# Kernel tuning notes

Hardware: AMD Instinct MI355X
Metric: run time of the kernel (lower is better)

The kernel has to match this reference:

```python
import jax, jax.numpy as jnp
import numpy as np

B, S, D = 8, 2048, 512

def setup_inputs() -> dict:
    key = jax.random.key(0)
    ks = jax.random.split(key, 9)
    sc = 1.0 / np.sqrt(D)
    return {
        "x": jax.random.normal(ks[0], (B, S, D), jnp.float32),
        "Wq": jax.random.normal(ks[1], (D, D), jnp.float32) * sc,
        "bq": jax.random.normal(ks[2], (D,), jnp.float32) * sc,
        "Wv": jax.random.normal(ks[3], (D, D), jnp.float32) * sc,
        "bv": jax.random.normal(ks[4], (D,), jnp.float32) * sc,
        "Wr": jax.random.normal(ks[5], (D, D), jnp.float32) * sc,
        "br": jax.random.normal(ks[6], (D,), jnp.float32) * sc,
        "Wl": jax.random.normal(ks[7], (1, D), jnp.float32) * sc,
        "bl": jax.random.normal(ks[8], (1,), jnp.float32) * sc,
    }

def reference(x, Wq, bq, Wv, bv, Wr, br, Wl, bl):
    # projections (torch Linear: x @ W.T + b)
    q = x @ Wq.T + bq          # [B,S,D]
    v = x @ Wv.T + bv          # [B,S,D]
    r = x @ Wr.T + br          # [B,S,D]
    # scores = Q @ V^T, softmax over dim=1 (the query/row axis!)
    scores = jnp.einsum("bsd,btd->bst", q, v)   # [B,S,S]
    attn = jax.nn.softmax(scores, axis=1)
    emb = jnp.einsum("bst,btd->bsd", attn, r)   # [B,S,D]
    pooled = emb.sum(axis=1)                    # [B,D]
    out = pooled @ Wl.T + bl                    # [B,1]
    return jax.nn.sigmoid(out)
```

## Files before the change

kernel.cpp:

```cpp
#include <hip/hip_runtime.h>
#include <math.h>

#define B 8
#define S 2048
#define D 512


#define CH 64
#define ROWS (S / CH)
#define DCH 32
#define DROWS (D / DCH)

__global__ void zero_ws_kernel(float* ws, int n) {
    int i = blockIdx.x * blockDim.x + threadIdx.x;
    if (i < n) ws[i] = 0.0f;
}

__global__ void colsum_x_kernel(const float4* __restrict__ x, float* __restrict__ xs) {
    int blk = blockIdx.x;
    int b = blk / CH;
    int ch = blk % CH;
    int tid = threadIdx.x;
    const float4* p = x + (size_t)(b * S + ch * ROWS) * (D / 4) + tid;
    float4 acc = {0.f, 0.f, 0.f, 0.f};
#pragma unroll
    for (int i = 0; i < ROWS; ++i) {
        float4 v = p[(size_t)i * (D / 4)];
        acc.x += v.x; acc.y += v.y; acc.z += v.z; acc.w += v.w;
    }
    float* dst = xs + b * D + tid * 4;
    atomicAdd(dst + 0, acc.x);
    atomicAdd(dst + 1, acc.y);
    atomicAdd(dst + 2, acc.z);
    atomicAdd(dst + 3, acc.w);
}

__global__ void wlwr_kernel(const float4* __restrict__ Wr, const float* __restrict__ Wl,
                            float* __restrict__ wcomb) {
    int ch = blockIdx.x;
    int tid = threadIdx.x;
    float4 acc = {0.f, 0.f, 0.f, 0.f};
#pragma unroll
    for (int i = 0; i < DROWS; ++i) {
        int d = ch * DROWS + i;
        float wl = Wl[d];
        float4 v = Wr[(size_t)d * (D / 4) + tid];
        acc.x += wl * v.x; acc.y += wl * v.y; acc.z += wl * v.z; acc.w += wl * v.w;
    }
    float* dst = wcomb + tid * 4;
    atomicAdd(dst + 0, acc.x);
    atomicAdd(dst + 1, acc.y);
    atomicAdd(dst + 2, acc.z);
    atomicAdd(dst + 3, acc.w);
}

__global__ void final_kernel(const float* __restrict__ xs, const float* __restrict__ wcomb,
                             const float* __restrict__ Wl, const float* __restrict__ br,
                             const float* __restrict__ bl, float* __restrict__ out) {
    int w = threadIdx.x >> 6;
    int l = threadIdx.x & 63;
    float s = 0.f, wb = 0.f;
#pragma unroll
    for (int k = 0; k < D / 64; ++k) {
        int e = l + 64 * k;
        s  += xs[w * D + e] * wcomb[e];
        wb += Wl[e] * br[e];
    }
#pragma unroll
    for (int off = 32; off > 0; off >>= 1) {
        s  += __shfl_down(s, off);
        wb += __shfl_down(wb, off);
    }
    if (l == 0) {
        float logit = s + (float)S * wb + bl[0];
        out[w] = 1.0f / (1.0f + expf(-logit));
    }
}

extern "C" void kernel_launch(void* const* d_in, const int* in_sizes, int n_in,
                              void* d_out, int out_size, void* d_ws, size_t ws_size,
                              hipStream_t stream) {
    const float* x  = (const float*)d_in[0];
    const float* Wr = (const float*)d_in[5];
    const float* br = (const float*)d_in[6];
    const float* Wl = (const float*)d_in[7];
    const float* bl = (const float*)d_in[8];
    float* out = (float*)d_out;

    float* xs    = (float*)d_ws;
    float* wcomb = xs + B * D;
    const int ws_floats = B * D + D;

    zero_ws_kernel<<<(ws_floats + 255) / 256, 256, 0, stream>>>((float*)d_ws, ws_floats);
    colsum_x_kernel<<<B * CH, 128, 0, stream>>>((const float4*)x, xs);
    wlwr_kernel<<<DCH, 128, 0, stream>>>((const float4*)Wr, Wl, wcomb);
    final_kernel<<<1, 512, 0, stream>>>(xs, wcomb, Wl, br, bl, out);
}
```

Before: 101.5 us.

## Merge column-sum and Wl·Wr kernels, replace atomics with partial buffers

The x column-sum and the Wl·Wr combination now run as one launch, with blocks choosing their role by index. Each block writes its partial sums to a workspace buffer instead of using float atomics, so the zeroing kernel is no longer needed. Stage 1 uses 256 threads split into two halves that are combined through shared memory. The final kernel now uses one block per batch and reduces the partials itself. Launch count drops from four to two, at the cost of extra workspace traffic for the partials.

```diff
diff --git a/kernel.cpp b/kernel.cpp
--- a/kernel.cpp
+++ b/kernel.cpp
@@ -8,72 +8,85 @@
 
 #define CH 64
 #define ROWS (S / CH)
-#define DCH 32
-#define DROWS (D / DCH)
+#define WBLK 32
+#define WROWS (D / WBLK)
 
-__global__ void zero_ws_kernel(float* ws, int n) {
-    int i = blockIdx.x * blockDim.x + threadIdx.x;
-    if (i < n) ws[i] = 0.0f;
+__global__ __launch_bounds__(256) void stage1(const float4* __restrict__ x,
+                                              const float4* __restrict__ Wr,
+                                              const float* __restrict__ Wl,
+                                              float4* __restrict__ px,
+                                              float4* __restrict__ pw) {
+    __shared__ float4 sbuf[128];
+    const int tid  = threadIdx.x;
+    const int col  = tid & 127;
+    const int half = tid >> 7;
+    const int blk  = blockIdx.x;
+    float4 acc = {0.f, 0.f, 0.f, 0.f};
+
+    if (blk < B * CH) {
+        const int b = blk / CH, ch = blk % CH;
+        const float4* p = x + (size_t)(b * S + ch * ROWS + half) * (D / 4) + col;
+#pragma unroll
+        for (int i = 0; i < ROWS; i += 2) {
+            float4 v = p[(size_t)i * (D / 4)];
+            acc.x += v.x; acc.y += v.y; acc.z += v.z; acc.w += v.w;
+        }
+    } else {
+        const int j = blk - B * CH;
+#pragma unroll
+        for (int i = 0; i < WROWS; i += 2) {
+            int d = j * WROWS + i + half;
+            float wl = Wl[d];
+            float4 v = Wr[(size_t)d * (D / 4) + col];
+            acc.x += wl * v.x; acc.y += wl * v.y; acc.z += wl * v.z; acc.w += wl * v.w;
+        }
+    }
+
+    if (half) sbuf[col] = acc;
+    __syncthreads();
+    if (!half) {
+        float4 o = sbuf[col];
+        acc.x += o.x; acc.y += o.y; acc.z += o.z; acc.w += o.w;
+        if (blk < B * CH) px[(size_t)blk * (D / 4) + col] = acc;
+        else              pw[(size_t)(blk - B * CH) * (D / 4) + col] = acc;
+    }
 }
 
-__global__ void colsum_x_kernel(const float4* __restrict__ x, float* __restrict__ xs) {
-    int blk = blockIdx.x;
-    int b = blk / CH;
-    int ch = blk % CH;
-    int tid = threadIdx.x;
-    const float4* p = x + (size_t)(b * S + ch * ROWS) * (D / 4) + tid;
-    float4 acc = {0.f, 0.f, 0.f, 0.f};
+__global__ __launch_bounds__(512) void stage2(const float* __restrict__ px,
+                                              const float* __restrict__ pw,
+                                              const float* __restrict__ Wl,
+                                              const float* __restrict__ br,
+                                              const float* __restrict__ bl,
+                                              float* __restrict__ out) {
+    const int b = blockIdx.x;
+    const int e = threadIdx.x;
+
+    float wsum = 0.f;
 #pragma unroll
-    for (int i = 0; i < ROWS; ++i) {
-        float4 v = p[(size_t)i * (D / 4)];
-        acc.x += v.x; acc.y += v.y; acc.z += v.z; acc.w += v.w;
-    }
-    float* dst = xs + b * D + tid * 4;
-    atomicAdd(dst + 0, acc.x);
-    atomicAdd(dst + 1, acc.y);
-    atomicAdd(dst + 2, acc.z);
-    atomicAdd(dst + 3, acc.w);
-}
+    for (int j = 0; j < WBLK; ++j) wsum += pw[j * D + e];
 
-__global__ void wlwr_kernel(const float4* __restrict__ Wr, const float* __restrict__ Wl,
-                            float* __restrict__ wcomb) {
-    int ch = blockIdx.x;
-    int tid = threadIdx.x;
-    float4 acc = {0.f, 0.f, 0.f, 0.f};
+    float xsum = 0.f;
 #pragma unroll
-    for (int i = 0; i < DROWS; ++i) {
-        int d = ch * DROWS + i;
-        float wl = Wl[d];
-        float4 v = Wr[(size_t)d * (D / 4) + tid];
-        acc.x += wl * v.x; acc.y += wl * v.y; acc.z += wl * v.z; acc.w += wl * v.w;
-    }
-    float* dst = wcomb + tid * 4;
-    atomicAdd(dst + 0, acc.x);
-    atomicAdd(dst + 1, acc.y);
-    atomicAdd(dst + 2, acc.z);
-    atomicAdd(dst + 3, acc.w);
-}
+    for (int ch = 0; ch < CH; ++ch) xsum += px[((size_t)b * CH + ch) * D + e];
 
-__global__ void final_kernel(const float* __restrict__ xs, const float* __restrict__ wcomb,
-                             const float* __restrict__ Wl, const float* __restrict__ br,
-                             const float* __restrict__ bl, float* __restrict__ out) {
-    int w = threadIdx.x >> 6;
-    int l = threadIdx.x & 63;
-    float s = 0.f, wb = 0.f;
-#pragma unroll
-    for (int k = 0; k < D / 64; ++k) {
-        int e = l + 64 * k;
-        s  += xs[w * D + e] * wcomb[e];
-        wb += Wl[e] * br[e];
-    }
+    float val = xsum * wsum;
+    float wb  = Wl[e] * br[e];
+
 #pragma unroll
     for (int off = 32; off > 0; off >>= 1) {
-        s  += __shfl_down(s, off);
-        wb += __shfl_down(wb, off);
+        val += __shfl_down(val, off);
+        wb  += __shfl_down(wb, off);
     }
-    if (l == 0) {
-        float logit = s + (float)S * wb + bl[0];
-        out[w] = 1.0f / (1.0f + expf(-logit));
+    __shared__ float sv[8], sw[8];
+    const int w = e >> 6, l = e & 63;
+    if (l == 0) { sv[w] = val; sw[w] = wb; }
+    __syncthreads();
+    if (e == 0) {
+        float v = 0.f, wbt = 0.f;
+#pragma unroll
+        for (int i = 0; i < 8; ++i) { v += sv[i]; wbt += sw[i]; }
+        float logit = v + (float)S * wbt + bl[0];
+        out[b] = 1.0f / (1.0f + expf(-logit));
     }
 }
 
@@ -87,12 +100,10 @@
     const float* bl = (const float*)d_in[8];
     float* out = (float*)d_out;
 
-    float* xs    = (float*)d_ws;
-    float* wcomb = xs + B * D;
-    const int ws_floats = B * D + D;
+    float* px = (float*)d_ws;
+    float* pw = px + (size_t)B * CH * D;
 
-    zero_ws_kernel<<<(ws_floats + 255) / 256, 256, 0, stream>>>((float*)d_ws, ws_floats);
-    colsum_x_kernel<<<B * CH, 128, 0, stream>>>((const float4*)x, xs);
-    wlwr_kernel<<<DCH, 128, 0, stream>>>((const float4*)Wr, Wl, wcomb);
-    final_kernel<<<1, 512, 0, stream>>>(xs, wcomb, Wl, br, bl, out);
+    stage1<<<B * CH + WBLK, 256, 0, stream>>>((const float4*)x, (const float4*)Wr, Wl,
+                                              (float4*)px, (float4*)pw);
+    stage2<<<B, 512, 0, stream>>>(px, pw, Wl, br, bl, out);
 }
```

After: 92.56 us, median of 2. -8.8%, faster.
